# Optimization experiments

Hardware: AMD Instinct MI355X
Metric: run time of the kernel (lower is better)

## Reference

```python
import jax, jax.numpy as jnp
import numpy as np

B, NATOM, NFEAT, NNEIGH = 8, 512, 42, 100
NTYPES, NPT = 2, 256          # atoms per type
H1, H2 = 64, 32               # nNodes per hidden layer (nLayers=3)
EI_MEAN = (-3.5, -4.2)        # itype_Ei_mean output-bias init


def _mlp(x, w0, b0, w1, b1, w2, b2):
    # tanh MLP: [*, NFEAT] -> [*, 1]  (FCNet forward, energy head)
    h = jnp.tanh(x @ w0.T + b0)
    h = jnp.tanh(h @ w1.T + b1)
    return h @ w2.T + b2


def _ei_all(image, W0, b0, W1, b1, W2, b2):
    # per-type slices of the atom axis, concatenated back: [B, NATOM, 1]
    outs = []
    for t in range(NTYPES):
        x = image[:, t * NPT:(t + 1) * NPT]
        outs.append(_mlp(x, W0[t], b0[t], W1[t], b1[t], W2[t], b2[t]))
    return jnp.concatenate(outs, axis=1)


def setup_inputs() -> dict:
    key = jax.random.key(0)
    ks = jax.random.split(key, 9)
    image = jax.random.normal(ks[0], (B, NATOM, NFEAT), jnp.float32)
    dfeat = jax.random.normal(ks[1], (B, NATOM, NNEIGH, NFEAT, 3), jnp.float32)
    neighbor = jax.random.randint(ks[2], (B, NATOM, NNEIGH), 0, NATOM + 1, jnp.int64)
    natoms_img = jnp.tile(jnp.array([[NATOM, NPT, NPT]], jnp.int64), (B, 1))
    # Xavier-ish per-type stacked MLP params
    W0 = jax.random.normal(ks[3], (NTYPES, H1, NFEAT), jnp.float32) * np.float32(np.sqrt(2.0 / (NFEAT + H1)))
    b0 = jnp.zeros((NTYPES, H1), jnp.float32)
    W1 = jax.random.normal(ks[4], (NTYPES, H2, H1), jnp.float32) * np.float32(np.sqrt(2.0 / (H1 + H2)))
    b1 = jnp.zeros((NTYPES, H2), jnp.float32)
    W2 = jax.random.normal(ks[5], (NTYPES, 1, H2), jnp.float32) * np.float32(np.sqrt(2.0 / (H2 + 1)))
    b2 = jnp.array(EI_MEAN, jnp.float32).reshape(NTYPES, 1)
    return {"image": image, "dfeat": dfeat, "neighbor": neighbor, "natoms_img": natoms_img,
            "W0": W0, "b0": b0, "W1": W1, "b1": b1, "W2": W2, "b2": b2}


def reference(image, dfeat, neighbor, natoms_img, W0, b0, W1, b1, W2, b2):
    del natoms_img  # per-type split is static (NPT atoms per type)
    Ei = _ei_all(image, W0, b0, W1, b1, W2, b2)   # [B, NATOM, 1]
    Etot = Ei.sum(axis=1)                          # [B, 1]
    # dEi/d(feature) of every atom (== torch.autograd.grad(Ei.sum(), image))
    dE = jax.grad(lambda im: _ei_all(im, W0, b0, W1, b1, W2, b2).sum())(image)  # [B, NATOM, NFEAT]
    # fortran-style padded table: row 0 per batch is zeros (neighbor index 0 = none)
    padded = jnp.concatenate([jnp.zeros((B, 1, NFEAT), dE.dtype), dE], axis=1)  # [B, NATOM+1, NFEAT]
    idx = neighbor.reshape(B, NATOM * NNEIGH)
    gathered = jnp.take_along_axis(padded, idx[:, :, None], axis=1)
    gathered = gathered.reshape(B, NATOM, NNEIGH, NFEAT)
    # Force[b,a,k] = sum_{n,f} dEi_neighbors[b,a,n,f] * dfeat[b,a,n,f,k]
    Force = jnp.einsum('banf,banfk->bak', gathered, dfeat)  # [B, NATOM, 3]
    return Etot, Ei, Force
```

## Files before the change

### kernel.cpp

```cpp
#include <hip/hip_runtime.h>
#include <hip/hip_bf16.h>

#define BQ 8
#define NATOM 512
#define NFEAT 42
#define NNEIGH 100
#define H1 64
#define H2 32

typedef float vf4 __attribute__((ext_vector_type(4)));

#define WS_DE 0
#define WS_EI (BQ * (NATOM + 1) * NFEAT)

__global__ __launch_bounds__(256) void k_ei(
    const float* __restrict__ image,
    const float* __restrict__ W0, const float* __restrict__ b0,
    const float* __restrict__ W1, const float* __restrict__ b1,
    const float* __restrict__ W2, const float* __restrict__ b2,
    float* __restrict__ dE,
    float* __restrict__ eiF,
    float* __restrict__ outEi)
{
    __shared__ float W0s[H1 * 43];
    __shared__ float W1s[H2 * 65];
    __shared__ float W2s[H2];
    __shared__ float b0s[H1];
    __shared__ float b1s[H2];
    __shared__ float xs[4][44];
    __shared__ float h0s[4][H1];
    __shared__ float g1s[4][H2];
    __shared__ float g0s[4][H1];

    const int tid  = threadIdx.x;
    const int w    = tid >> 6;
    const int lane = tid & 63;
    const int ga   = blockIdx.x * 4 + w;
    const int b    = ga >> 9;
    const int t    = (blockIdx.x >> 6) & 1;

    for (int e = tid; e < H1 * NFEAT; e += 256) {
        int r = e / NFEAT, c = e - r * NFEAT;
        W0s[r * 43 + c] = W0[t * (H1 * NFEAT) + e];
    }
    for (int e = tid; e < H2 * H1; e += 256) {
        int r = e >> 6, c = e & 63;
        W1s[r * 65 + c] = W1[t * (H2 * H1) + e];
    }
    if (tid < H2) { W2s[tid] = W2[t * H2 + tid]; b1s[tid] = b1[t * H2 + tid]; }
    if (tid >= 64 && tid < 128) b0s[tid - 64] = b0[t * H1 + (tid - 64)];
    if (lane < NFEAT) xs[w][lane] = image[(size_t)ga * NFEAT + lane];
    __syncthreads();

    float s = b0s[lane];
    #pragma unroll
    for (int f = 0; f < NFEAT; ++f) s = fmaf(W0s[lane * 43 + f], xs[w][f], s);
    const float h0 = tanhf(s);
    h0s[w][lane] = h0;
    __syncthreads();

    const int k = lane & 31;
    s = b1s[k];
    #pragma unroll
    for (int j = 0; j < H1; ++j) s = fmaf(W1s[k * 65 + j], h0s[w][j], s);
    const float h1 = tanhf(s);

    float p = W2s[k] * h1;
    p += __shfl_down(p, 16, 64);
    p += __shfl_down(p, 8, 64);
    p += __shfl_down(p, 4, 64);
    p += __shfl_down(p, 2, 64);
    p += __shfl_down(p, 1, 64);
    if (lane == 0) {
        float y = p + b2[t];
        eiF[ga]   = y;
        outEi[ga] = y;
    }

    const float g1 = W2s[k] * (1.0f - h1 * h1);
    if (lane < H2) g1s[w][lane] = g1;
    __syncthreads();

    s = 0.0f;
    #pragma unroll
    for (int kk = 0; kk < H2; ++kk) s = fmaf(g1s[w][kk], W1s[kk * 65 + lane], s);
    const float g0 = s * (1.0f - h0 * h0);
    g0s[w][lane] = g0;
    __syncthreads();

    if (lane < NFEAT) {
        s = 0.0f;
        #pragma unroll
        for (int j = 0; j < H1; ++j) s = fmaf(g0s[w][j], W0s[j * 43 + lane], s);
        dE[((size_t)b * (NATOM + 1) + (ga & 511) + 1) * NFEAT + lane] = s;
    }

    if ((blockIdx.x & 127) == 0 && tid < NFEAT)
        dE[(size_t)(blockIdx.x >> 7) * (NATOM + 1) * NFEAT + tid] = 0.0f;
}

__global__ __launch_bounds__(256) void k_force(
    const float* __restrict__ dfeat,
    const int* __restrict__ neighbor,
    const float* __restrict__ dE,
    const float* __restrict__ eiF,
    float* __restrict__ out)
{
    __shared__ float g[NNEIGH * NFEAT];
    __shared__ int nb[NNEIGH];
    __shared__ float red[12];

    const int ba  = blockIdx.x;
    const int b   = ba >> 9;
    const int tid = threadIdx.x;

    if (tid < NNEIGH) nb[tid] = neighbor[(size_t)ba * NNEIGH + tid];
    __syncthreads();

    const float* __restrict__ dEb = dE + (size_t)b * (NATOM + 1) * NFEAT;
    for (int e = tid; e < NNEIGH * NFEAT; e += 256) {
        int n = e / NFEAT;
        int f = e - n * NFEAT;
        g[e] = dEb[(size_t)nb[n] * NFEAT + f];
    }
    __syncthreads();

    const int tid3 = tid % 3;
    int  qm[3];
    bool sel1[3], sel2[3];
    #pragma unroll
    for (int m = 0; m < 3; ++m) {
        int j = tid + 256 * m;
        int r = (tid3 + m) % 3;
        qm[m]   = j + (j - r) / 3;
        sel1[m] = (r < 2);
        sel2[m] = (r == 0);
    }

    const float* __restrict__ df = dfeat + (size_t)ba * (NNEIGH * NFEAT * 3);
    const vf4* __restrict__ df4 = (const vf4*)df;

    float c0 = 0.f, c1 = 0.f, c2 = 0.f;
    #pragma unroll
    for (int k = 0; k < 12; ++k) {
        const int m = k % 3;
        vf4 v = __builtin_nontemporal_load(df4 + tid + 256 * k);
        int q = qm[m] + (k / 3) * 1024;
        float gq = g[q], gq1 = g[q + 1];
        float s1 = sel1[m] ? gq : gq1;
        float s2 = sel2[m] ? gq : gq1;
        float p0 = gq * v.x, p1 = s1 * v.y, p2 = s2 * v.z, p3 = gq1 * v.w;
        if (m == 0) { c0 += p0; c1 += p1; c2 += p2; c0 += p3; }
        if (m == 1) { c1 += p0; c2 += p1; c0 += p2; c1 += p3; }
        if (m == 2) { c2 += p0; c0 += p1; c1 += p2; c2 += p3; }
    }
    if (tid < 3150 - 3072) {
        vf4 v = __builtin_nontemporal_load(df4 + tid + 3072);
        int q = qm[0] + 4096;
        float gq = g[q], gq1 = g[q + 1];
        float s1 = sel1[0] ? gq : gq1;
        float s2 = sel2[0] ? gq : gq1;
        c0 += gq * v.x; c1 += s1 * v.y; c2 += s2 * v.z; c0 += gq1 * v.w;
    }

    float a0, a1, a2;
    if (tid3 == 0)      { a0 = c0; a1 = c1; a2 = c2; }
    else if (tid3 == 1) { a1 = c0; a2 = c1; a0 = c2; }
    else                { a2 = c0; a0 = c1; a1 = c2; }

    #pragma unroll
    for (int off = 32; off > 0; off >>= 1) {
        a0 += __shfl_down(a0, off, 64);
        a1 += __shfl_down(a1, off, 64);
        a2 += __shfl_down(a2, off, 64);
    }
    const int wave = tid >> 6, lane = tid & 63;
    if (lane == 0) { red[wave * 3] = a0; red[wave * 3 + 1] = a1; red[wave * 3 + 2] = a2; }
    __syncthreads();
    if (tid < 3) {
        float s = red[tid] + red[3 + tid] + red[6 + tid] + red[9 + tid];
        out[8 + BQ * NATOM + (size_t)ba * 3 + tid] = s;
    }

    if (blockIdx.x == 0) {
        for (int bb = wave * 2; bb < wave * 2 + 2; ++bb) {
            float s = 0.f;
            for (int i = lane; i < NATOM; i += 64) s += eiF[bb * NATOM + i];
            #pragma unroll
            for (int off = 32; off > 0; off >>= 1) s += __shfl_down(s, off, 64);
            if (lane == 0) out[bb] = s;
        }
    }
}

extern "C" void kernel_launch(void* const* d_in, const int* in_sizes, int n_in,
                              void* d_out, int out_size, void* d_ws, size_t ws_size,
                              hipStream_t stream)
{
    const float* image    = (const float*)d_in[0];
    const float* dfeat    = (const float*)d_in[1];
    const int*   neighbor = (const int*)d_in[2];
    const float* W0 = (const float*)d_in[4];
    const float* b0 = (const float*)d_in[5];
    const float* W1 = (const float*)d_in[6];
    const float* b1 = (const float*)d_in[7];
    const float* W2 = (const float*)d_in[8];
    const float* b2 = (const float*)d_in[9];

    float* wsf  = (float*)d_ws;
    float* dE   = wsf + WS_DE;
    float* eiF  = wsf + WS_EI;
    float* out  = (float*)d_out;

    hipLaunchKernelGGL(k_ei, dim3(1024), dim3(256), 0, stream,
                       image, W0, b0, W1, b1, W2, b2, dE, eiF, out + 8);
    hipLaunchKernelGGL(k_force, dim3(4096), dim3(256), 0, stream,
                       dfeat, neighbor, dE, eiF, out);
}
```

Baseline: 294.3 us.

## Process two atoms per wave in MLP kernel and prefetch dfeat before gather

The energy/gradient kernel now has each wave handle two atoms, so each weight value read from shared memory serves two FMAs and the grid halves, spreading the per-block weight staging over more work. The force kernel issues the first four dfeat vector loads before the neighbor-gather barrier, so the HBM stream overlaps the neighbor index load and the dE gather. This raises register pressure in both kernels and changes the block-to-type and batch-zeroing index math.

```diff
diff --git a/kernel.cpp b/kernel.cpp
--- a/kernel.cpp
+++ b/kernel.cpp
@@ -1,5 +1,4 @@
 #include <hip/hip_runtime.h>
-#include <hip/hip_bf16.h>
 
 #define BQ 8
 #define NATOM 512
@@ -27,17 +26,18 @@
     __shared__ float W2s[H2];
     __shared__ float b0s[H1];
     __shared__ float b1s[H2];
-    __shared__ float xs[4][44];
-    __shared__ float h0s[4][H1];
-    __shared__ float g1s[4][H2];
-    __shared__ float g0s[4][H1];
-
-    const int tid  = threadIdx.x;
-    const int w    = tid >> 6;
-    const int lane = tid & 63;
-    const int ga   = blockIdx.x * 4 + w;
-    const int b    = ga >> 9;
-    const int t    = (blockIdx.x >> 6) & 1;
+    __shared__ float xs[8][44];
+    __shared__ float h0s[4][2][H1];
+    __shared__ float g1s[4][2][H2];
+    __shared__ float g0s[4][2][H1];
+
+    const int tid   = threadIdx.x;
+    const int w     = tid >> 6;
+    const int lane  = tid & 63;
+    const int gbase = blockIdx.x * 8;
+    const int ga0   = gbase + w * 2;
+    const int b     = ga0 >> 9;
+    const int t     = (blockIdx.x >> 5) & 1;
 
     for (int e = tid; e < H1 * NFEAT; e += 256) {
         int r = e / NFEAT, c = e - r * NFEAT;
@@ -49,54 +49,77 @@
     }
     if (tid < H2) { W2s[tid] = W2[t * H2 + tid]; b1s[tid] = b1[t * H2 + tid]; }
     if (tid >= 64 && tid < 128) b0s[tid - 64] = b0[t * H1 + (tid - 64)];
-    if (lane < NFEAT) xs[w][lane] = image[(size_t)ga * NFEAT + lane];
-    __syncthreads();
-
-    float s = b0s[lane];
-    #pragma unroll
-    for (int f = 0; f < NFEAT; ++f) s = fmaf(W0s[lane * 43 + f], xs[w][f], s);
-    const float h0 = tanhf(s);
-    h0s[w][lane] = h0;
+    for (int e = tid; e < 8 * NFEAT; e += 256) {
+        int n = e / NFEAT, f = e - n * NFEAT;
+        xs[n][f] = image[(size_t)(gbase + n) * NFEAT + f];
+    }
+    __syncthreads();
+
+    float s0 = b0s[lane], s1 = b0s[lane];
+    #pragma unroll
+    for (int f = 0; f < NFEAT; ++f) {
+        float w0 = W0s[lane * 43 + f];
+        s0 = fmaf(w0, xs[w * 2][f], s0);
+        s1 = fmaf(w0, xs[w * 2 + 1][f], s1);
+    }
+    const float h0a = tanhf(s0), h0b = tanhf(s1);
+    h0s[w][0][lane] = h0a;
+    h0s[w][1][lane] = h0b;
     __syncthreads();
 
     const int k = lane & 31;
-    s = b1s[k];
-    #pragma unroll
-    for (int j = 0; j < H1; ++j) s = fmaf(W1s[k * 65 + j], h0s[w][j], s);
-    const float h1 = tanhf(s);
-
-    float p = W2s[k] * h1;
-    p += __shfl_down(p, 16, 64);
-    p += __shfl_down(p, 8, 64);
-    p += __shfl_down(p, 4, 64);
-    p += __shfl_down(p, 2, 64);
-    p += __shfl_down(p, 1, 64);
+    s0 = b1s[k]; s1 = b1s[k];
+    #pragma unroll
+    for (int j = 0; j < H1; ++j) {
+        float w1 = W1s[k * 65 + j];
+        s0 = fmaf(w1, h0s[w][0][j], s0);
+        s1 = fmaf(w1, h0s[w][1][j], s1);
+    }
+    const float h1a = tanhf(s0), h1b = tanhf(s1);
+
+    float p0 = W2s[k] * h1a;
+    float p1 = W2s[k] * h1b;
+    #pragma unroll
+    for (int off = 16; off > 0; off >>= 1) {
+        p0 += __shfl_down(p0, off, 64);
+        p1 += __shfl_down(p1, off, 64);
+    }
     if (lane == 0) {
-        float y = p + b2[t];
-        eiF[ga]   = y;
-        outEi[ga] = y;
-    }
-
-    const float g1 = W2s[k] * (1.0f - h1 * h1);
-    if (lane < H2) g1s[w][lane] = g1;
-    __syncthreads();
-
-    s = 0.0f;
-    #pragma unroll
-    for (int kk = 0; kk < H2; ++kk) s = fmaf(g1s[w][kk], W1s[kk * 65 + lane], s);
-    const float g0 = s * (1.0f - h0 * h0);
-    g0s[w][lane] = g0;
+        float y0 = p0 + b2[t], y1 = p1 + b2[t];
+        eiF[ga0]       = y0;  eiF[ga0 + 1]   = y1;
+        outEi[ga0]     = y0;  outEi[ga0 + 1] = y1;
+    }
+
+    const float h1s = (lane < 32) ? h1a : h1b;
+    g1s[w][lane >> 5][k] = W2s[k] * (1.0f - h1s * h1s);
+    __syncthreads();
+
+    s0 = 0.0f; s1 = 0.0f;
+    #pragma unroll
+    for (int kk = 0; kk < H2; ++kk) {
+        float w1 = W1s[kk * 65 + lane];
+        s0 = fmaf(g1s[w][0][kk], w1, s0);
+        s1 = fmaf(g1s[w][1][kk], w1, s1);
+    }
+    g0s[w][0][lane] = s0 * (1.0f - h0a * h0a);
+    g0s[w][1][lane] = s1 * (1.0f - h0b * h0b);
     __syncthreads();
 
     if (lane < NFEAT) {
-        s = 0.0f;
+        s0 = 0.0f; s1 = 0.0f;
         #pragma unroll
-        for (int j = 0; j < H1; ++j) s = fmaf(g0s[w][j], W0s[j * 43 + lane], s);
-        dE[((size_t)b * (NATOM + 1) + (ga & 511) + 1) * NFEAT + lane] = s;
-    }
-
-    if ((blockIdx.x & 127) == 0 && tid < NFEAT)
-        dE[(size_t)(blockIdx.x >> 7) * (NATOM + 1) * NFEAT + tid] = 0.0f;
+        for (int j = 0; j < H1; ++j) {
+            float w0 = W0s[j * 43 + lane];
+            s0 = fmaf(g0s[w][0][j], w0, s0);
+            s1 = fmaf(g0s[w][1][j], w0, s1);
+        }
+        size_t base = ((size_t)b * (NATOM + 1) + (ga0 & 511) + 1) * NFEAT + lane;
+        dE[base]         = s0;
+        dE[base + NFEAT] = s1;
+    }
+
+    if ((blockIdx.x & 63) == 0 && tid < NFEAT)
+        dE[(size_t)(blockIdx.x >> 6) * (NATOM + 1) * NFEAT + tid] = 0.0f;
 }
 
 __global__ __launch_bounds__(256) void k_force(
@@ -114,7 +137,16 @@
     const int b   = ba >> 9;
     const int tid = threadIdx.x;
 
+    const float* __restrict__ df = dfeat + (size_t)ba * (NNEIGH * NFEAT * 3);
+    const vf4* __restrict__ df4 = (const vf4*)df;
+
     if (tid < NNEIGH) nb[tid] = neighbor[(size_t)ba * NNEIGH + tid];
+
+    vf4 pf0 = __builtin_nontemporal_load(df4 + tid);
+    vf4 pf1 = __builtin_nontemporal_load(df4 + tid + 256);
+    vf4 pf2 = __builtin_nontemporal_load(df4 + tid + 512);
+    vf4 pf3 = __builtin_nontemporal_load(df4 + tid + 768);
+
     __syncthreads();
 
     const float* __restrict__ dEb = dE + (size_t)b * (NATOM + 1) * NFEAT;
@@ -137,14 +169,16 @@
         sel2[m] = (r == 0);
     }
 
-    const float* __restrict__ df = dfeat + (size_t)ba * (NNEIGH * NFEAT * 3);
-    const vf4* __restrict__ df4 = (const vf4*)df;
-
     float c0 = 0.f, c1 = 0.f, c2 = 0.f;
     #pragma unroll
     for (int k = 0; k < 12; ++k) {
         const int m = k % 3;
-        vf4 v = __builtin_nontemporal_load(df4 + tid + 256 * k);
+        vf4 v;
+        if      (k == 0) v = pf0;
+        else if (k == 1) v = pf1;
+        else if (k == 2) v = pf2;
+        else if (k == 3) v = pf3;
+        else             v = __builtin_nontemporal_load(df4 + tid + 256 * k);
         int q = qm[m] + (k / 3) * 1024;
         float gq = g[q], gq1 = g[q + 1];
         float s1 = sel1[m] ? gq : gq1;
@@ -212,7 +246,7 @@
     float* eiF  = wsf + WS_EI;
     float* out  = (float*)d_out;
 
-    hipLaunchKernelGGL(k_ei, dim3(1024), dim3(256), 0, stream,
+    hipLaunchKernelGGL(k_ei, dim3(512), dim3(256), 0, stream,
                        image, W0, b0, W1, b1, W2, b2, dE, eiF, out + 8);
     hipLaunchKernelGGL(k_force, dim3(4096), dim3(256), 0, stream,
                        dfeat, neighbor, dE, eiF, out);
```

Result: no change. 295.0 us (+0.2%).
